# Performance work log

Hardware: AMD Instinct MI355X
Metric: run time of the kernel (lower is better)

## Reference

```python
import jax, jax.numpy as jnp
import numpy as np

B, N, D, H = 8, 128, 512, 16
DK = D // H


def setup_inputs() -> dict:
    key = jax.random.key(0)
    ks = jax.random.split(key, 10)
    s = 1.0 / np.sqrt(D)
    return {
        "query_node": jax.random.normal(ks[0], (B, N, D), jnp.float32),
        "value_node": jax.random.normal(ks[1], (B, N, D), jnp.float32),
        "key_edge": jax.random.normal(ks[2], (B, N, N, D), jnp.float32) * 0.1,
        "adj_matrix": jax.random.uniform(ks[3], (B, N, N), jnp.float32),  # nonneg distance matrix
        "mask": jnp.ones((B, N), jnp.int32),
        "Wq": jax.random.normal(ks[4], (D, D), jnp.float32) * s,
        "bq": jnp.zeros((D,), jnp.float32),
        "Wk": jax.random.normal(ks[5], (D, D), jnp.float32) * s,
        "bk": jnp.zeros((D,), jnp.float32),
        "Wv": jax.random.normal(ks[6], (D, D), jnp.float32) * s,
        "bv": jnp.zeros((D,), jnp.float32),
        "Wo": jax.random.normal(ks[7], (D, D), jnp.float32) * s,
        "bo": jnp.zeros((D,), jnp.float32),
        "We": jax.random.normal(ks[8], (D, D), jnp.float32) * s,
        "be": jnp.zeros((D,), jnp.float32),
        "att_lambda": jnp.asarray(0.1, jnp.float32),
    }


def reference(query_node, value_node, key_edge, adj_matrix, mask,
              Wq, bq, Wk, bk, Wv, bv, Wo, bo, We, be, att_lambda):
    b, n, d = query_node.shape
    mask1 = mask[:, None, :]  # [b,1,n], broadcasts over rows like mask.repeat(1,n,1)
    # attenuated distance matrix -> kernel (softmax(-x)); masked entries -> +inf -> 0 weight
    adj = att_lambda * adj_matrix
    adj = jnp.where(mask1 == 0, jnp.inf, adj)
    adj = jax.nn.softmax(-adj, axis=-1)  # [b,n,n]
    # projections
    q = (query_node @ Wq + bq).reshape(b, n, H, DK).transpose(0, 2, 1, 3)      # [b,h,n,dk]
    k = (key_edge @ Wk + bk).reshape(b, n, n, H, DK).transpose(0, 3, 1, 2, 4)  # [b,h,n,n,dk]
    v = (value_node @ Wv + bv).reshape(b, n, H, DK).transpose(0, 2, 1, 3)      # [b,h,n,dk]
    scale = 1.0 / jnp.sqrt(jnp.asarray(DK, q.dtype))
    out_scores = jnp.einsum('bhmd,bhmnd->bhmn', q, k) * scale
    in_scores = jnp.einsum('bhnd,bhmnd->bhnm', q, k) * scale
    kmask = (mask1[:, :, None, :] == 0)  # [b,1,1,n]; mask value only depends on last axis
    neg = jnp.asarray(-jnp.inf, q.dtype)
    out_attn = jax.nn.softmax(jnp.where(kmask, neg, out_scores), axis=-1)
    in_attn = jax.nn.softmax(jnp.where(kmask, neg, in_scores), axis=-1)
    # message = out_attn + in_attn - diag_embed(diagonal(out_attn))
    diag = jnp.einsum('bhii->bhi', out_attn)
    idx = jnp.arange(n)
    message = (out_attn + in_attn).at[:, :, idx, idx].add(-diag)
    message = message * adj[:, None]  # adjacency gating, [b,h,n,n]
    node_hidden = jnp.einsum('bhmn,bhnd->bhmd', message, v)  # [b,h,n,dk]
    edge_hidden = message[..., None] * k                      # [b,h,m,n,dk]
    x = node_hidden.transpose(0, 2, 1, 3).reshape(b, n, d)
    e = edge_hidden.transpose(0, 2, 3, 1, 4).reshape(b, n, n, d)
    return (x @ Wo + bo, e @ We + be)
```

## Files before the change

kernel.cpp:

```cpp
#include <hip/hip_runtime.h>
#include <math.h>


using f32x4  = __attribute__((ext_vector_type(4))) float;
using bf16x8 = __attribute__((ext_vector_type(8))) short;

typedef const __attribute__((address_space(1))) unsigned int* gas_u32p;
typedef __attribute__((address_space(3))) unsigned int* las_u32p;

__device__ __forceinline__ void gll16(const void* gsrc, void* ldst) {
  __builtin_amdgcn_global_load_lds((gas_u32p)gsrc, (las_u32p)ldst, 16, 0, 0);
}

__device__ __forceinline__ unsigned short f2bf(float f) {
  union { float f; unsigned u; } v; v.f = f;
  unsigned u = v.u;
  u += 0x7FFFu + ((u >> 16) & 1u);
  return (unsigned short)(u >> 16);
}
__device__ __forceinline__ float bf2f(unsigned short h) {
  union { unsigned u; float f; } v; v.u = ((unsigned)h) << 16; return v.f;
}
__device__ __forceinline__ unsigned pack2(float lo, float hi) {
  union { float f; unsigned u; } a, b; a.f = lo; b.f = hi;
  return __builtin_amdgcn_perm(b.u + 0x8000u, a.u + 0x8000u, 0x07060302u);
}
__device__ __forceinline__ unsigned scale_pair(unsigned u, float mv) {
  union { unsigned u; float f; } lo, hi;
  lo.u = u << 16; hi.u = u & 0xFFFF0000u;
  float a = lo.f * mv, b = hi.f * mv;
  return pack2(a, b);
}

__global__ __launch_bounds__(256) void wt_kernel(const float* __restrict__ W,
                                                 unsigned short* __restrict__ WT) {
  __shared__ unsigned short T[64][72];
  int tile = blockIdx.x;
  int ti = tile >> 3, tj = tile & 7;
  int k0 = ti * 64, n0 = tj * 64;
  int t = threadIdx.x;
  int r = t >> 2, cq = (t & 3) * 16;
  const float* src = W + (size_t)(k0 + r) * 512 + n0 + cq;
#pragma unroll
  for (int j = 0; j < 16; ++j) T[r][cq + j] = f2bf(src[j]);
  __syncthreads();
  int c = t >> 2, rq = (t & 3) * 16;
  unsigned short* dst = WT + (size_t)(n0 + c) * 512 + k0 + rq;
#pragma unroll
  for (int j = 0; j < 16; ++j) dst[j] = T[rq + j][c];
}

__global__ __launch_bounds__(256) void adj_kernel(const float* __restrict__ adjm,
                                                  const int* __restrict__ mask,
                                                  const float* __restrict__ lam_p,
                                                  float* __restrict__ adjsm) {
  int row = blockIdx.x * 4 + (threadIdx.x >> 6);
  int lane = threadIdx.x & 63;
  int b = row >> 7;
  float lam = lam_p[0];
  const float* src = adjm + (size_t)row * 128;
  int m0 = mask[b * 128 + lane], m1 = mask[b * 128 + 64 + lane];
  float x0 = m0 ? -lam * src[lane] : -INFINITY;
  float x1 = m1 ? -lam * src[64 + lane] : -INFINITY;
  float mx = fmaxf(x0, x1);
#pragma unroll
  for (int o = 32; o; o >>= 1) mx = fmaxf(mx, __shfl_xor(mx, o));
  float e0 = __expf(x0 - mx), e1 = __expf(x1 - mx);
  float s = e0 + e1;
#pragma unroll
  for (int o = 32; o; o >>= 1) s += __shfl_xor(s, o);
  float inv = 1.0f / s;
  adjsm[(size_t)row * 128 + lane] = e0 * inv;
  adjsm[(size_t)row * 128 + 64 + lane] = e1 * inv;
}

__global__ __launch_bounds__(256) void gemm_kernel(const float* __restrict__ A,
                                                   const unsigned short* __restrict__ WT,
                                                   const float* __restrict__ bias,
                                                   float* __restrict__ C) {
  __shared__ unsigned short As[128 * 40];
  __shared__ unsigned short Bs[128 * 40];
  const int bid = blockIdx.x;
  const int rb = bid >> 2, cb = bid & 3;
  const int t = threadIdx.x;
  const int row0 = rb * 128, col0 = cb * 128;
  const int wave = t >> 6, lane = t & 63;
  const int wm = wave >> 1, wn = wave & 1;
  const int l15 = lane & 15, q4 = lane >> 4;
  const int arow = t >> 1, ahalf = t & 1;

  f32x4 acc[4][4];
#pragma unroll
  for (int i = 0; i < 4; ++i)
#pragma unroll
    for (int j = 0; j < 4; ++j)
#pragma unroll
      for (int r = 0; r < 4; ++r) acc[i][j][r] = 0.0f;

  for (int ki = 0; ki < 16; ++ki) {
    const int k0 = ki * 32;
    {
      const float* src = A + (size_t)(row0 + arow) * 512 + k0 + ahalf * 16;
      f32x4 v0 = *(const f32x4*)(src + 0);
      f32x4 v1 = *(const f32x4*)(src + 4);
      f32x4 v2 = *(const f32x4*)(src + 8);
      f32x4 v3 = *(const f32x4*)(src + 12);
      union { unsigned short u[16]; uint4 q[2]; } w;
#pragma unroll
      for (int j = 0; j < 4; ++j) {
        w.u[j] = f2bf(v0[j]); w.u[4 + j] = f2bf(v1[j]);
        w.u[8 + j] = f2bf(v2[j]); w.u[12 + j] = f2bf(v3[j]);
      }
      unsigned short* d = &As[arow * 40 + ahalf * 16];
      *(uint4*)d = w.q[0];
      *(uint4*)(d + 8) = w.q[1];
    }
    {
      const unsigned short* src = WT + (size_t)(col0 + arow) * 512 + k0 + ahalf * 16;
      uint4 p0 = *(const uint4*)src;
      uint4 p1 = *(const uint4*)(src + 8);
      unsigned short* d = &Bs[arow * 40 + ahalf * 16];
      *(uint4*)d = p0;
      *(uint4*)(d + 8) = p1;
    }
    __syncthreads();
    bf16x8 af[4], bfr[4];
#pragma unroll
    for (int mt = 0; mt < 4; ++mt)
      af[mt] = *(const bf16x8*)&As[(wm * 64 + mt * 16 + l15) * 40 + q4 * 8];
#pragma unroll
    for (int nt = 0; nt < 4; ++nt)
      bfr[nt] = *(const bf16x8*)&Bs[(wn * 64 + nt * 16 + l15) * 40 + q4 * 8];
#pragma unroll
    for (int mt = 0; mt < 4; ++mt)
#pragma unroll
      for (int nt = 0; nt < 4; ++nt)
        acc[mt][nt] = __builtin_amdgcn_mfma_f32_16x16x32_bf16(af[mt], bfr[nt], acc[mt][nt], 0, 0, 0);
    __syncthreads();
  }
#pragma unroll
  for (int mt = 0; mt < 4; ++mt) {
#pragma unroll
    for (int nt = 0; nt < 4; ++nt) {
      int gcol = col0 + wn * 64 + nt * 16 + l15;
      float bv = bias[gcol];
#pragma unroll
      for (int r = 0; r < 4; ++r) {
        int grow = row0 + wm * 64 + mt * 16 + q4 * 4 + r;
        C[(size_t)grow * 512 + gcol] = acc[mt][nt][r] + bv;
      }
    }
  }
}

template <int AMODE>
__global__ __launch_bounds__(256, 2) void gemm2_kernel(
    const void* __restrict__ Aptr, const unsigned short* __restrict__ WT,
    const float* __restrict__ bias, void* __restrict__ Cptr,
    const float* __restrict__ msg) {
  constexpr int ABYTES = (AMODE == 2) ? 8192 : 16384;
  __shared__ char smem[ABYTES + 16384 + 512];
  float* Asf = (float*)smem;
  unsigned short* Abf = (unsigned short*)smem;
  unsigned short* Bs = (unsigned short*)(smem + ABYTES);
  float* ms = (float*)(smem + ABYTES + 16384);

  const int bid = blockIdx.x;
  const int rb = bid >> 1, cb = bid & 1;
  const int row0 = rb * 128, col0 = cb * 256;
  const int t = threadIdx.x;
  const int wave = t >> 6, lane = t & 63;
  const int wm = wave >> 1, wn = wave & 1;
  const int l15 = lane & 15, q4 = lane >> 4;

  size_t msbase = 0;
  if (AMODE == 2) {
    int b = row0 >> 14, m = (row0 >> 7) & 127;
    msbase = (size_t)(b * 16) * 16384 + m * 128;
  }

  f32x4 acc[4][8];
#pragma unroll
  for (int i = 0; i < 4; ++i)
#pragma unroll
    for (int j = 0; j < 8; ++j)
#pragma unroll
      for (int r = 0; r < 4; ++r) acc[i][j][r] = 0.0f;

  for (int ki = 0; ki < 16; ++ki) {
    const int k0 = ki * 32;
    if (AMODE != 2) {
      const float* A = (const float*)Aptr;
#pragma unroll
      for (int c = 0; c < 4; ++c) {
        int ar = (wave * 4 + c) * 8 + (lane >> 3);
        int p = (lane & 7) >> 1, h = lane & 1;
        int gcol = ((p ^ (ar & 3)) << 3) + (h << 2);
        gll16(A + (size_t)(row0 + ar) * 512 + k0 + gcol,
              Asf + (size_t)(wave * 4 + c) * 256);
      }
    } else {
      const unsigned short* A = (const unsigned short*)Aptr;
#pragma unroll
      for (int c = 0; c < 2; ++c) {
        int ar = (wave * 2 + c) * 16 + (lane >> 2);
        int gq = (lane & 3) ^ (ar & 3);
        gll16(A + (size_t)(row0 + ar) * 512 + k0 + gq * 8,
              Abf + (size_t)(wave * 2 + c) * 512);
      }
      if (t < 128) ms[t] = msg[msbase + (size_t)ki * 16384 + t];
    }
#pragma unroll
    for (int c = 0; c < 4; ++c) {
      int br = (wave * 4 + c) * 16 + (lane >> 2);
      int gq = (lane & 3) ^ (br & 3);
      gll16(WT + (size_t)(col0 + br) * 512 + k0 + gq * 8,
            Bs + (size_t)(wave * 4 + c) * 512);
    }
    __syncthreads();

    bf16x8 bfr[8], af[4];
#pragma unroll
    for (int nt = 0; nt < 8; ++nt) {
      int brow = wn * 128 + nt * 16 + l15;
      bfr[nt] = *(const bf16x8*)&Bs[brow * 32 + ((q4 ^ (brow & 3)) << 3)];
    }
    if (AMODE != 2) {
#pragma unroll
      for (int mt = 0; mt < 4; ++mt) {
        int arow = wm * 64 + mt * 16 + l15;
        const float* ap = &Asf[arow * 32 + ((q4 ^ (arow & 3)) << 3)];
        f32x4 v0 = *(const f32x4*)ap;
        f32x4 v1 = *(const f32x4*)(ap + 4);
        union { unsigned d[4]; bf16x8 v; } u;
        u.d[0] = pack2(v0[0], v0[1]); u.d[1] = pack2(v0[2], v0[3]);
        u.d[2] = pack2(v1[0], v1[1]); u.d[3] = pack2(v1[2], v1[3]);
        af[mt] = u.v;
      }
    } else {
#pragma unroll
      for (int mt = 0; mt < 4; ++mt) {
        int arow = wm * 64 + mt * 16 + l15;
        union { unsigned d[4]; bf16x8 v; } u;
        u.v = *(const bf16x8*)&Abf[arow * 32 + ((q4 ^ (arow & 3)) << 3)];
        float mv = ms[arow];
        u.d[0] = scale_pair(u.d[0], mv);
        u.d[1] = scale_pair(u.d[1], mv);
        u.d[2] = scale_pair(u.d[2], mv);
        u.d[3] = scale_pair(u.d[3], mv);
        af[mt] = u.v;
      }
    }
#pragma unroll
    for (int mt = 0; mt < 4; ++mt)
#pragma unroll
      for (int nt = 0; nt < 8; ++nt)
        acc[mt][nt] = __builtin_amdgcn_mfma_f32_16x16x32_bf16(af[mt], bfr[nt], acc[mt][nt], 0, 0, 0);
    __syncthreads();
  }
#pragma unroll
  for (int mt = 0; mt < 4; ++mt) {
#pragma unroll
    for (int nt = 0; nt < 8; ++nt) {
      int gcol = col0 + wn * 128 + nt * 16 + l15;
      float bv = bias[gcol];
#pragma unroll
      for (int r = 0; r < 4; ++r) {
        int grow = row0 + wm * 64 + mt * 16 + q4 * 4 + r;
        float val = acc[mt][nt][r] + bv;
        if (AMODE == 1)
          ((unsigned short*)Cptr)[(size_t)grow * 512 + gcol] = f2bf(val);
        else
          ((float*)Cptr)[(size_t)grow * 512 + gcol] = val;
      }
    }
  }
}

__global__ __launch_bounds__(512) void scores_kernel(const unsigned short* __restrict__ Kbf,
                                                     const float* __restrict__ qw,
                                                     const int* __restrict__ mask,
                                                     float* __restrict__ sout,
                                                     float* __restrict__ sinT) {
  __shared__ float lso[16 * 9];
  __shared__ float lsi[16 * 9];
  const int bm = blockIdx.x;
  const int b = bm >> 7;
  const int t = threadIdx.x;
  const int wave = t >> 6, lane = t & 63;
  const float scale = 0.17677669529663687f;
  const int maskm = mask[bm];
  float qmr[8];
  {
    const float* qp = qw + (size_t)bm * 512 + lane * 8;
    f32x4 a = *(const f32x4*)qp, bq = *(const f32x4*)(qp + 4);
#pragma unroll
    for (int j = 0; j < 4; ++j) { qmr[j] = a[j]; qmr[4 + j] = bq[j]; }
  }
  for (int it = 0; it < 16; ++it) {
    int n = it * 8 + wave;
    const unsigned short* kp = Kbf + ((size_t)bm * 128 + n) * 512 + lane * 8;
    uint4 kv = *(const uint4*)kp;
    const float* qnp = qw + ((size_t)(b * 128 + n)) * 512 + lane * 8;
    f32x4 qa = *(const f32x4*)qnp, qb = *(const f32x4*)(qnp + 4);
    float qnr[8];
#pragma unroll
    for (int j = 0; j < 4; ++j) { qnr[j] = qa[j]; qnr[4 + j] = qb[j]; }
    unsigned vals[4] = {kv.x, kv.y, kv.z, kv.w};
    float so = 0.f, si = 0.f;
#pragma unroll
    for (int j = 0; j < 4; ++j) {
      float k0 = bf2f((unsigned short)(vals[j] & 0xFFFFu));
      float k1 = bf2f((unsigned short)(vals[j] >> 16));
      so += qmr[2 * j] * k0 + qmr[2 * j + 1] * k1;
      si += qnr[2 * j] * k0 + qnr[2 * j + 1] * k1;
    }
    so += __shfl_xor(so, 1); so += __shfl_xor(so, 2);
    si += __shfl_xor(si, 1); si += __shfl_xor(si, 2);
    int maskn = mask[b * 128 + n];
    if ((lane & 3) == 0) {
      int h = lane >> 2;
      lso[h * 9 + wave] = maskn ? so * scale : -INFINITY;
      lsi[h * 9 + wave] = maskm ? si * scale : -INFINITY;
    }
    __syncthreads();
    if (t < 256) {
      int sel = t >> 7, u = t & 127, h = u >> 3, w = u & 7;
      float v = sel ? lsi[h * 9 + w] : lso[h * 9 + w];
      float* dst = sel ? sinT : sout;
      dst[((size_t)(b * 16 + h) * 128 + (bm & 127)) * 128 + it * 8 + w] = v;
    }
    __syncthreads();
  }
}

__global__ __launch_bounds__(256) void tr128_kernel(const float* __restrict__ src,
                                                    float* __restrict__ dst) {
  __shared__ float T[64][65];
  int bid = blockIdx.x;
  int mat = bid >> 2, tile = bid & 3;
  int ti = tile >> 1, tj = tile & 1;
  const float* s = src + (size_t)mat * 16384;
  float* d = dst + (size_t)mat * 16384;
  int t = threadIdx.x;
  int r = t >> 2, cq = (t & 3) * 16;
#pragma unroll
  for (int j = 0; j < 16; ++j) T[r][cq + j] = s[(size_t)(ti * 64 + r) * 128 + tj * 64 + cq + j];
  __syncthreads();
  int c = t >> 2, rq = (t & 3) * 16;
#pragma unroll
  for (int j = 0; j < 16; ++j) d[(size_t)(tj * 64 + c) * 128 + ti * 64 + rq + j] = T[rq + j][c];
}

__global__ __launch_bounds__(256) void rsm_kernel(float* __restrict__ x) {
  int row = blockIdx.x * 4 + (threadIdx.x >> 6);
  int lane = threadIdx.x & 63;
  float* p = x + (size_t)row * 128;
  float a0 = p[lane], a1 = p[lane + 64];
  float mx = fmaxf(a0, a1);
#pragma unroll
  for (int o = 32; o; o >>= 1) mx = fmaxf(mx, __shfl_xor(mx, o));
  float e0 = __expf(a0 - mx), e1 = __expf(a1 - mx);
  float s = e0 + e1;
#pragma unroll
  for (int o = 32; o; o >>= 1) s += __shfl_xor(s, o);
  float inv = 1.0f / s;
  p[lane] = e0 * inv;
  p[lane + 64] = e1 * inv;
}

__global__ __launch_bounds__(256) void msg_kernel(const float* __restrict__ outat,
                                                  float* __restrict__ inat_msg,
                                                  const float* __restrict__ adjsm) {
  size_t idx = (size_t)blockIdx.x * 256 + threadIdx.x;
  int c = (int)(idx & 127), r = (int)((idx >> 7) & 127);
  int bh = (int)(idx >> 14), b = bh >> 4;
  float o = outat[idx], in = inat_msg[idx];
  float mv = (r == c) ? in : (o + in);
  mv *= adjsm[((size_t)b * 128 + r) * 128 + c];
  inat_msg[idx] = mv;
}

__global__ __launch_bounds__(256) void node_kernel(const float* __restrict__ msg,
                                                   const float* __restrict__ vw,
                                                   float* __restrict__ xpre) {
  __shared__ float V[128 * 36];
  __shared__ float Mg[64 * 132];
  int bid = blockIdx.x;
  int bh = bid >> 1, half = bid & 1;
  int b = bh >> 4, h = bh & 15;
  int t = threadIdx.x;
#pragma unroll
  for (int i = 0; i < 16; ++i) {
    int idx = t + i * 256;
    int j = idx >> 5, dk = idx & 31;
    V[j * 36 + dk] = vw[((size_t)b * 128 + j) * 512 + h * 32 + dk];
  }
  const float* mrow = msg + (size_t)bh * 16384 + (size_t)half * 64 * 128;
#pragma unroll
  for (int i = 0; i < 32; ++i) {
    int idx = t + i * 256;
    int r = idx >> 7, c = idx & 127;
    Mg[r * 132 + c] = mrow[idx];
  }
  __syncthreads();
  int il = t >> 2, d0 = (t & 3) * 8;
  float acc[8] = {0, 0, 0, 0, 0, 0, 0, 0};
  for (int j = 0; j < 128; ++j) {
    float mv = Mg[il * 132 + j];
#pragma unroll
    for (int d = 0; d < 8; ++d) acc[d] += mv * V[j * 36 + d0 + d];
  }
  float* xp = xpre + ((size_t)b * 128 + half * 64 + il) * 512 + h * 32 + d0;
#pragma unroll
  for (int d = 0; d < 8; ++d) xp[d] = acc[d];
}

extern "C" void kernel_launch(void* const* d_in, const int* in_sizes, int n_in,
                              void* d_out, int out_size, void* d_ws, size_t ws_size,
                              hipStream_t stream) {
  const float* q_node   = (const float*)d_in[0];
  const float* v_node   = (const float*)d_in[1];
  const float* key_edge = (const float*)d_in[2];
  const float* adjm     = (const float*)d_in[3];
  const int*   mask     = (const int*)d_in[4];
  const float* Wq = (const float*)d_in[5];
  const float* bq = (const float*)d_in[6];
  const float* Wk = (const float*)d_in[7];
  const float* bk = (const float*)d_in[8];
  const float* Wv = (const float*)d_in[9];
  const float* bv = (const float*)d_in[10];
  const float* Wo = (const float*)d_in[11];
  const float* bo = (const float*)d_in[12];
  const float* We = (const float*)d_in[13];
  const float* be = (const float*)d_in[14];
  const float* lam = (const float*)d_in[15];

  char* ws = (char*)d_ws;
  unsigned short* Kbf   = (unsigned short*)(ws);
  float* sout  = (float*)(ws + 134217728);
  float* sinT  = (float*)(ws + 142606336);
  float* msgb  = (float*)(ws + 150994944);
  float* adjsm = (float*)(ws + 159383552);
  float* qw    = (float*)(ws + 159907840);
  float* vw    = (float*)(ws + 162004992);
  float* xpre  = (float*)(ws + 164102144);
  unsigned short* WqT = (unsigned short*)(ws + 166199296);
  unsigned short* WkT = WqT + 262144;
  unsigned short* WvT = WkT + 262144;
  unsigned short* WoT = WvT + 262144;
  unsigned short* WeT = WoT + 262144;

  float* out_x = (float*)d_out;
  float* out_e = out_x + 524288;

  wt_kernel<<<64, 256, 0, stream>>>(Wq, WqT);
  wt_kernel<<<64, 256, 0, stream>>>(Wk, WkT);
  wt_kernel<<<64, 256, 0, stream>>>(Wv, WvT);
  wt_kernel<<<64, 256, 0, stream>>>(Wo, WoT);
  wt_kernel<<<64, 256, 0, stream>>>(We, WeT);
  adj_kernel<<<256, 256, 0, stream>>>(adjm, mask, lam, adjsm);

  gemm_kernel<<<32, 256, 0, stream>>>(q_node, WqT, bq, qw);
  gemm_kernel<<<32, 256, 0, stream>>>(v_node, WvT, bv, vw);
  gemm2_kernel<1><<<2048, 256, 0, stream>>>(key_edge, WkT, bk, Kbf, nullptr);

  scores_kernel<<<1024, 512, 0, stream>>>(Kbf, qw, mask, sout, sinT);
  tr128_kernel<<<512, 256, 0, stream>>>(sinT, msgb);
  rsm_kernel<<<4096, 256, 0, stream>>>(sout);
  rsm_kernel<<<4096, 256, 0, stream>>>(msgb);
  msg_kernel<<<8192, 256, 0, stream>>>(sout, msgb, adjsm);
  node_kernel<<<256, 256, 0, stream>>>(msgb, vw, xpre);

  gemm_kernel<<<32, 256, 0, stream>>>(xpre, WoT, bo, out_x);
  gemm2_kernel<2><<<2048, 256, 0, stream>>>(Kbf, WeT, be, out_e, msgb);
}
```

Before: 807.7 us.

## Multi-stage LDS pipeline for big edge GEMMs with preloaded message scales

```diff
diff --git a/kernel.cpp b/kernel.cpp
--- a/kernel.cpp
+++ b/kernel.cpp
@@ -158,12 +158,11 @@
     const void* __restrict__ Aptr, const unsigned short* __restrict__ WT,
     const float* __restrict__ bias, void* __restrict__ Cptr,
     const float* __restrict__ msg) {
+  constexpr int DEPTH  = (AMODE == 2) ? 3 : 2;
   constexpr int ABYTES = (AMODE == 2) ? 8192 : 16384;
-  __shared__ char smem[ABYTES + 16384 + 512];
-  float* Asf = (float*)smem;
-  unsigned short* Abf = (unsigned short*)smem;
-  unsigned short* Bs = (unsigned short*)(smem + ABYTES);
-  float* ms = (float*)(smem + ABYTES + 16384);
+  constexpr int STAGEB = ABYTES + 16384;
+  extern __shared__ char smem[];
+  float* Msh = (float*)(smem + DEPTH * STAGEB);
 
   const int bid = blockIdx.x;
   const int rb = bid >> 1, cb = bid & 1;
@@ -173,12 +172,6 @@
   const int wm = wave >> 1, wn = wave & 1;
   const int l15 = lane & 15, q4 = lane >> 4;
 
-  size_t msbase = 0;
-  if (AMODE == 2) {
-    int b = row0 >> 14, m = (row0 >> 7) & 127;
-    msbase = (size_t)(b * 16) * 16384 + m * 128;
-  }
-
   f32x4 acc[4][8];
 #pragma unroll
   for (int i = 0; i < 4; ++i)
@@ -187,10 +180,12 @@
 #pragma unroll
       for (int r = 0; r < 4; ++r) acc[i][j][r] = 0.0f;
 
-  for (int ki = 0; ki < 16; ++ki) {
+  auto STAGE = [&](int ki, int s) {
     const int k0 = ki * 32;
+    char* sa = smem + s * STAGEB;
     if (AMODE != 2) {
       const float* A = (const float*)Aptr;
+      float* Asf = (float*)sa;
 #pragma unroll
       for (int c = 0; c < 4; ++c) {
         int ar = (wave * 4 + c) * 8 + (lane >> 3);
@@ -201,6 +196,7 @@
       }
     } else {
       const unsigned short* A = (const unsigned short*)Aptr;
+      unsigned short* Abf = (unsigned short*)sa;
 #pragma unroll
       for (int c = 0; c < 2; ++c) {
         int ar = (wave * 2 + c) * 16 + (lane >> 2);
@@ -208,17 +204,46 @@
         gll16(A + (size_t)(row0 + ar) * 512 + k0 + gq * 8,
               Abf + (size_t)(wave * 2 + c) * 512);
       }
-      if (t < 128) ms[t] = msg[msbase + (size_t)ki * 16384 + t];
-    }
+    }
+    unsigned short* Bsb = (unsigned short*)(sa + ABYTES);
 #pragma unroll
     for (int c = 0; c < 4; ++c) {
       int br = (wave * 4 + c) * 16 + (lane >> 2);
       int gq = (lane & 3) ^ (br & 3);
       gll16(WT + (size_t)(col0 + br) * 512 + k0 + gq * 8,
-            Bs + (size_t)(wave * 4 + c) * 512);
-    }
+            Bsb + (size_t)(wave * 4 + c) * 512);
+    }
+  };
+
+  if (AMODE == 2) {
+    int b = row0 >> 14, m = (row0 >> 7) & 127;
+    size_t msbase = (size_t)(b * 16) * 16384 + (size_t)m * 128;
+    int h = t >> 4, n8 = (t & 15) * 8;
+    const float* mp = msg + msbase + (size_t)h * 16384 + n8;
+    f32x4 m0 = *(const f32x4*)mp;
+    f32x4 m1 = *(const f32x4*)(mp + 4);
+    *(f32x4*)&Msh[h * 128 + n8] = m0;
+    *(f32x4*)&Msh[h * 128 + n8 + 4] = m1;
     __syncthreads();
-
+  }
+
+  STAGE(0, 0);
+  if (DEPTH == 3) STAGE(1, 1);
+
+#pragma unroll
+  for (int ki = 0; ki < 16; ++ki) {
+    if (DEPTH == 3) {
+      if (ki < 15) asm volatile("s_waitcnt vmcnt(6)" ::: "memory");
+      else         asm volatile("s_waitcnt vmcnt(0)" ::: "memory");
+    } else {
+      asm volatile("s_waitcnt vmcnt(0)" ::: "memory");
+    }
+    __builtin_amdgcn_s_barrier();
+    __builtin_amdgcn_sched_barrier(0);
+    if (ki + DEPTH - 1 < 16) STAGE(ki + DEPTH - 1, (ki + DEPTH - 1) % DEPTH);
+
+    char* sc = smem + (ki % DEPTH) * STAGEB;
+    unsigned short* Bs = (unsigned short*)(sc + ABYTES);
     bf16x8 bfr[8], af[4];
 #pragma unroll
     for (int nt = 0; nt < 8; ++nt) {
@@ -226,6 +251,7 @@
       bfr[nt] = *(const bf16x8*)&Bs[brow * 32 + ((q4 ^ (brow & 3)) << 3)];
     }
     if (AMODE != 2) {
+      float* Asf = (float*)sc;
 #pragma unroll
       for (int mt = 0; mt < 4; ++mt) {
         int arow = wm * 64 + mt * 16 + l15;
@@ -238,12 +264,13 @@
         af[mt] = u.v;
       }
     } else {
+      unsigned short* Abf = (unsigned short*)sc;
 #pragma unroll
       for (int mt = 0; mt < 4; ++mt) {
         int arow = wm * 64 + mt * 16 + l15;
         union { unsigned d[4]; bf16x8 v; } u;
         u.v = *(const bf16x8*)&Abf[arow * 32 + ((q4 ^ (arow & 3)) << 3)];
-        float mv = ms[arow];
+        float mv = Msh[ki * 128 + arow];
         u.d[0] = scale_pair(u.d[0], mv);
         u.d[1] = scale_pair(u.d[1], mv);
         u.d[2] = scale_pair(u.d[2], mv);
@@ -256,7 +283,6 @@
 #pragma unroll
       for (int nt = 0; nt < 8; ++nt)
         acc[mt][nt] = __builtin_amdgcn_mfma_f32_16x16x32_bf16(af[mt], bfr[nt], acc[mt][nt], 0, 0, 0);
-    __syncthreads();
   }
 #pragma unroll
   for (int mt = 0; mt < 4; ++mt) {
@@ -463,7 +489,7 @@
 
   gemm_kernel<<<32, 256, 0, stream>>>(q_node, WqT, bq, qw);
   gemm_kernel<<<32, 256, 0, stream>>>(v_node, WvT, bv, vw);
-  gemm2_kernel<1><<<2048, 256, 0, stream>>>(key_edge, WkT, bk, Kbf, nullptr);
+  gemm2_kernel<1><<<2048, 256, 65536, stream>>>(key_edge, WkT, bk, Kbf, nullptr);
 
   scores_kernel<<<1024, 512, 0, stream>>>(Kbf, qw, mask, sout, sinT);
   tr128_kernel<<<512, 256, 0, stream>>>(sinT, msgb);
@@ -473,5 +499,5 @@
   node_kernel<<<256, 256, 0, stream>>>(msgb, vw, xpre);
 
   gemm_kernel<<<32, 256, 0, stream>>>(xpre, WoT, bo, out_x);
-  gemm2_kernel<2><<<2048, 256, 0, stream>>>(Kbf, WeT, be, out_e, msgb);
-}
+  gemm2_kernel<2><<<2048, 256, 81920, stream>>>(Kbf, WeT, be, out_e, msgb);
+}
```

New measurement: 771.7 us. 4.5% less time.
